# Kernel optimization log

Measured on AMD Instinct MI355X. Metric: run time of the kernel, lower is better.

The kernel has to match this reference:

```python
import jax, jax.numpy as jnp
import numpy as np

N_NODES = 50000
N_EDGES = 800000
IN_FEATS = 64
HIDDEN = 64
NUM_CLASSES = 8


def setup_inputs() -> dict:
    key = jax.random.key(0)
    ks = jax.random.split(key, 6)
    embeds = jax.random.normal(ks[0], (N_NODES, IN_FEATS), dtype=jnp.float32)
    edge_index = jax.random.randint(ks[1], (2, N_EDGES), 0, N_NODES, dtype=jnp.int32)
    sc1 = 1.0 / np.sqrt(IN_FEATS)
    sc2 = 1.0 / np.sqrt(HIDDEN)
    W_l1 = jax.random.normal(ks[2], (IN_FEATS, HIDDEN), dtype=jnp.float32) * sc1
    b_l1 = jnp.zeros((HIDDEN,), dtype=jnp.float32)
    W_r1 = jax.random.normal(ks[3], (IN_FEATS, HIDDEN), dtype=jnp.float32) * sc1
    W_l2 = jax.random.normal(ks[4], (HIDDEN, NUM_CLASSES), dtype=jnp.float32) * sc2
    b_l2 = jnp.zeros((NUM_CLASSES,), dtype=jnp.float32)
    W_r2 = jax.random.normal(ks[5], (HIDDEN, NUM_CLASSES), dtype=jnp.float32) * sc2
    return {"embeds": embeds, "edge_index": edge_index,
            "W_l1": W_l1, "b_l1": b_l1, "W_r1": W_r1,
            "W_l2": W_l2, "b_l2": b_l2, "W_r2": W_r2}


def _sage_conv(x, src, dst, W_l, b_l, W_r):
    # PyG SAGEConv('mean'): lin_l(mean_{j->i} x_j) + lin_r(x_i); lin_r has no bias.
    msg = x[src]                                                   # [E, F] gather
    agg = jax.ops.segment_sum(msg, dst, num_segments=N_NODES)      # [N, F]
    deg = jax.ops.segment_sum(jnp.ones((src.shape[0],), x.dtype), dst,
                              num_segments=N_NODES)                # [N]
    agg = agg / jnp.maximum(deg, 1.0)[:, None]
    return agg @ W_l + b_l + x @ W_r


def reference(embeds, edge_index, W_l1, b_l1, W_r1, W_l2, b_l2, W_r2):
    src, dst = edge_index[0], edge_index[1]
    h = _sage_conv(embeds, src, dst, W_l1, b_l1, W_r1)
    # dropout between layers is identity at inference; source applies no ReLU
    h = _sage_conv(h, src, dst, W_l2, b_l2, W_r2)
    return h
```

## Files before the change

### kernel.cpp

```cpp
#include <hip/hip_runtime.h>
#include <hip/hip_bf16.h>
#include <cstddef>

#define N_FEATS 64
#define NBKT_SHIFT 8
#define EPB 4096
#define CAP 6144

typedef __attribute__((ext_vector_type(8))) short bf16x8;
typedef __attribute__((ext_vector_type(4))) float f32x4;

__device__ __forceinline__ unsigned f2bf(float f) {
    unsigned x = __float_as_uint(f);
    return (x + 0x7fffu + ((x >> 16) & 1u)) >> 16;
}

__global__ __launch_bounds__(256) void k_init(
        const float* __restrict__ Wl1, const float* __restrict__ bl1,
        const float* __restrict__ Wr1, const float* __restrict__ Wl2,
        const float* __restrict__ bl2, const float* __restrict__ Wr2,
        unsigned short* __restrict__ Wc, float* __restrict__ bvec,
        int* __restrict__ cursor, int nbkt) {
    int tid = threadIdx.x;
    int k = tid & 63, jg = tid >> 6;
    const float* W1 = (jg < 2) ? Wl1 : Wr1;
    const float* W2 = (jg & 1) ? Wr2 : Wl2;
    float acc[8] = {0.f,0.f,0.f,0.f,0.f,0.f,0.f,0.f};
    for (int m = 0; m < 64; ++m) {
        float w1 = W1[k * 64 + m];
        #pragma unroll
        for (int jj = 0; jj < 8; ++jj) acc[jj] += w1 * W2[m * 8 + jj];
    }
    #pragma unroll
    for (int jj = 0; jj < 8; ++jj)
        Wc[k * 32 + jg * 8 + jj] = (unsigned short)f2bf(acc[jj]);
    if (tid < 16) {
        const float* W2b = (tid < 8) ? Wl2 : Wr2;
        float a = 0.f;
        for (int m = 0; m < 64; ++m) a += bl1[m] * W2b[m * 8 + (tid & 7)];
        if (tid >= 8) a += bl2[tid - 8];
        bvec[tid] = a;
    }
    if (tid < nbkt) cursor[tid] = 0;
}

__global__ __launch_bounds__(256) void k_split_gemm(
        const int* __restrict__ src, const int* __restrict__ dst,
        int* __restrict__ cursor, unsigned* __restrict__ pairs,
        int nEdges, int nbkt, int nb1,
        const float* __restrict__ x,
        const unsigned short* __restrict__ Wc,
        const float* __restrict__ bvec,
        unsigned short* __restrict__ G,
        float* __restrict__ T,
        int nNodes, int nStrips) {
    __shared__ unsigned spr[EPB];
    __shared__ int lh[256];
    __shared__ int lcur[256];
    int tid = threadIdx.x, b = blockIdx.x;

    if (b < nb1) {
        lh[tid] = 0;
        __syncthreads();
        int base = b * EPB;
        int m = nEdges - base; if (m > EPB) m = EPB;
        for (int j = tid; j < m; j += 256) {
            unsigned d = (unsigned)dst[base + j];
            spr[j] = ((unsigned)src[base + j] << 16) | d;
            atomicAdd(&lh[d >> NBKT_SHIFT], 1);
        }
        __syncthreads();
        if (tid < nbkt) lcur[tid] = atomicAdd(&cursor[tid], lh[tid]);
        __syncthreads();
        for (int j = tid; j < m; j += 256) {
            unsigned pr = spr[j];
            unsigned d = pr & 0xffffu;
            int bkt = d >> NBKT_SHIFT;
            int pos = atomicAdd(&lcur[bkt], 1);
            if (pos < CAP)
                pairs[(size_t)bkt * CAP + pos] = ((pr >> 16) << 8) | (d & 255u);
        }
        return;
    }

    int w  = tid >> 6;
    int l  = tid & 63;
    int fc = l & 15;
    int kg = l >> 4;
    bf16x8 bf[2][2];
    #pragma unroll
    for (int ct = 0; ct < 2; ++ct)
        #pragma unroll
        for (int kh = 0; kh < 2; ++kh)
            #pragma unroll
            for (int i = 0; i < 8; ++i) {
                int k = kh * 32 + kg * 8 + i;
                bf[ct][kh][i] = (short)Wc[k * 32 + ct * 16 + fc];
            }
    float bias = bvec[fc];

    for (int strip = b - nb1; strip < nStrips; strip += gridDim.x - nb1) {
        int node0 = strip * 64;
        int arow = node0 + w * 16 + fc;
        int ar = (arow < nNodes) ? arow : (nNodes - 1);
        const float* xp = x + (size_t)ar * 64 + kg * 8;
        float4 xa = *(const float4*)(xp);
        float4 xb = *(const float4*)(xp + 4);
        float4 xc = *(const float4*)(xp + 32);
        float4 xd = *(const float4*)(xp + 36);
        bf16x8 a0, a1;
        a0[0]=(short)f2bf(xa.x); a0[1]=(short)f2bf(xa.y);
        a0[2]=(short)f2bf(xa.z); a0[3]=(short)f2bf(xa.w);
        a0[4]=(short)f2bf(xb.x); a0[5]=(short)f2bf(xb.y);
        a0[6]=(short)f2bf(xb.z); a0[7]=(short)f2bf(xb.w);
        a1[0]=(short)f2bf(xc.x); a1[1]=(short)f2bf(xc.y);
        a1[2]=(short)f2bf(xc.z); a1[3]=(short)f2bf(xc.w);
        a1[4]=(short)f2bf(xd.x); a1[5]=(short)f2bf(xd.y);
        a1[6]=(short)f2bf(xd.z); a1[7]=(short)f2bf(xd.w);

        f32x4 d0 = {0.f, 0.f, 0.f, 0.f};
        f32x4 d1 = {0.f, 0.f, 0.f, 0.f};
        d0 = __builtin_amdgcn_mfma_f32_16x16x32_bf16(a0, bf[0][0], d0, 0, 0, 0);
        d0 = __builtin_amdgcn_mfma_f32_16x16x32_bf16(a1, bf[0][1], d0, 0, 0, 0);
        d1 = __builtin_amdgcn_mfma_f32_16x16x32_bf16(a0, bf[1][0], d1, 0, 0, 0);
        d1 = __builtin_amdgcn_mfma_f32_16x16x32_bf16(a1, bf[1][1], d1, 0, 0, 0);

        #pragma unroll
        for (int r = 0; r < 4; ++r) {
            int node = node0 + w * 16 + kg * 4 + r;
            if (node < nNodes) {
                G[(size_t)node * 16 + fc] = (unsigned short)f2bf(d0[r]);
                T[(size_t)node * 16 + fc] = d1[r] + bias;
            }
        }
    }
}

__global__ __launch_bounds__(1024) void k_fsort_gather2(
        const unsigned* __restrict__ pairs,
        const int* __restrict__ cursor,
        const unsigned* __restrict__ G,
        const float* __restrict__ T,
        int* __restrict__ counts,
        int* __restrict__ offsets,
        unsigned short* __restrict__ sorted_src,
        unsigned* __restrict__ pbf,
        float* __restrict__ q,
        int nNodes, int nbkt) {
    __shared__ unsigned short ss[CAP];
    __shared__ int cntA[256];
    __shared__ int scanbuf[256];
    __shared__ int loff[256];
    __shared__ int cur[256];
    int tid = threadIdx.x, b = blockIdx.x;
    int bStart = b * CAP;
    int m = cursor[b]; if (m > CAP) m = CAP;

    if (tid < 256) cntA[tid] = 0;
    __syncthreads();
    for (int e = tid; e < m; e += 1024)
        atomicAdd(&cntA[pairs[bStart + e] & 255u], 1);
    __syncthreads();
    int v = 0;
    if (tid < 256) { v = cntA[tid]; scanbuf[tid] = v; }
    __syncthreads();
    for (int d = 1; d < 256; d <<= 1) {
        int t = (tid < 256 && tid >= d) ? scanbuf[tid - d] : 0;
        __syncthreads();
        if (tid < 256) scanbuf[tid] += t;
        __syncthreads();
    }
    if (tid < 256) {
        int excl = scanbuf[tid] - v;
        loff[tid] = excl;
        cur[tid] = excl;
        int node = (b << NBKT_SHIFT) + tid;
        if (node < nNodes) { counts[node] = v; offsets[node] = bStart + excl; }
    }
    __syncthreads();
    for (int e = tid; e < m; e += 1024) {
        unsigned pr = pairs[bStart + e];
        int pos = atomicAdd(&cur[pr & 255u], 1);
        unsigned short sv = (unsigned short)(pr >> 8);
        ss[pos] = sv;
        sorted_src[bStart + pos] = sv;
    }
    __syncthreads();

    int wave = tid >> 6, lane = tid & 63;
    int half = lane >> 5;
    int eg   = (lane >> 2) & 7;
    int t4   = lane & 3;
    const uint2* G2 = (const uint2*)G;

    #pragma unroll 1
    for (int it = 0; it < 8; ++it) {
        int nl = it * 32 + wave * 2 + half;
        int node = (b << NBKT_SHIFT) + nl;
        if (node >= nNodes) continue;
        int cnt_n = cntA[nl];
        int lo = loff[nl];

        float a0 = 0.f, a1 = 0.f, a2 = 0.f, a3 = 0.f;
        int id = (eg < cnt_n) ? (int)ss[lo + eg] : -1;
        for (int base = 0; base < cnt_n; base += 8) {
            int en = base + 8 + eg;
            int idn = (en < cnt_n) ? (int)ss[lo + en] : -1;
            if (id >= 0) {
                uint2 r = G2[(size_t)id * 4 + t4];
                a0 += __uint_as_float(r.x << 16);
                a1 += __uint_as_float(r.x & 0xffff0000u);
                a2 += __uint_as_float(r.y << 16);
                a3 += __uint_as_float(r.y & 0xffff0000u);
            }
            id = idn;
        }
        a0 += __shfl_xor(a0, 4);  a1 += __shfl_xor(a1, 4);
        a2 += __shfl_xor(a2, 4);  a3 += __shfl_xor(a3, 4);
        a0 += __shfl_xor(a0, 8);  a1 += __shfl_xor(a1, 8);
        a2 += __shfl_xor(a2, 8);  a3 += __shfl_xor(a3, 8);
        a0 += __shfl_xor(a0, 16); a1 += __shfl_xor(a1, 16);
        a2 += __shfl_xor(a2, 16); a3 += __shfl_xor(a3, 16);

        if (eg == 0) {
            float inv = 1.0f / fmaxf((float)cnt_n, 1.0f);
            float4 tv = *(const float4*)&T[(size_t)node * 16 + t4 * 4];
            float r0 = a0 * inv + tv.x;
            float r1 = a1 * inv + tv.y;
            float r2 = a2 * inv + tv.z;
            float r3 = a3 * inv + tv.w;
            if (t4 < 2) {
                uint2 o;
                o.x = f2bf(r0) | (f2bf(r1) << 16);
                o.y = f2bf(r2) | (f2bf(r3) << 16);
                *(uint2*)(pbf + (size_t)node * 4 + t4 * 2) = o;
            } else {
                float4 o; o.x = r0; o.y = r1; o.z = r2; o.w = r3;
                *(float4*)(q + (size_t)node * 8 + (t4 - 2) * 4) = o;
            }
        }
    }
}

__global__ __launch_bounds__(256) void k_final(
        const unsigned* __restrict__ pbf,
        const float* __restrict__ q,
        const int* __restrict__ counts,
        const int* __restrict__ offsets,
        const unsigned short* __restrict__ ss,
        float* __restrict__ out,
        int nNodes) {
    int tid  = threadIdx.x;
    int wave = tid >> 6, lane = tid & 63;
    int half = lane >> 5;
    int eg   = (lane >> 1) & 15;
    int t2   = lane & 1;
    int node = blockIdx.x * 8 + wave * 2 + half;
    if (node >= nNodes) return;
    int cnt = counts[node], off = offsets[node];
    const uint2* P2 = (const uint2*)pbf;

    float a0 = 0.f, a1 = 0.f, a2 = 0.f, a3 = 0.f;
    int id = (eg < cnt) ? (int)ss[off + eg] : -1;
    for (int base = 0; base < cnt; base += 16) {
        int en = base + 16 + eg;
        int idn = (en < cnt) ? (int)ss[off + en] : -1;
        if (id >= 0) {
            uint2 r = P2[(size_t)id * 2 + t2];
            a0 += __uint_as_float(r.x << 16);
            a1 += __uint_as_float(r.x & 0xffff0000u);
            a2 += __uint_as_float(r.y << 16);
            a3 += __uint_as_float(r.y & 0xffff0000u);
        }
        id = idn;
    }
    a0 += __shfl_xor(a0, 2);  a1 += __shfl_xor(a1, 2);
    a2 += __shfl_xor(a2, 2);  a3 += __shfl_xor(a3, 2);
    a0 += __shfl_xor(a0, 4);  a1 += __shfl_xor(a1, 4);
    a2 += __shfl_xor(a2, 4);  a3 += __shfl_xor(a3, 4);
    a0 += __shfl_xor(a0, 8);  a1 += __shfl_xor(a1, 8);
    a2 += __shfl_xor(a2, 8);  a3 += __shfl_xor(a3, 8);
    a0 += __shfl_xor(a0, 16); a1 += __shfl_xor(a1, 16);
    a2 += __shfl_xor(a2, 16); a3 += __shfl_xor(a3, 16);

    if (eg == 0) {
        float inv = 1.0f / fmaxf((float)cnt, 1.0f);
        float4 qv = *(const float4*)&q[(size_t)node * 8 + t2 * 4];
        float4 o;
        o.x = a0 * inv + qv.x; o.y = a1 * inv + qv.y;
        o.z = a2 * inv + qv.z; o.w = a3 * inv + qv.w;
        *(float4*)(out + (size_t)node * 8 + t2 * 4) = o;
    }
}

static inline size_t align256(size_t v) { return (v + 255) & ~(size_t)255; }

extern "C" void kernel_launch(void* const* d_in, const int* in_sizes, int n_in,
                              void* d_out, int out_size, void* d_ws, size_t ws_size,
                              hipStream_t stream) {
    const float* embeds = (const float*)d_in[0];
    const int*   ei     = (const int*)d_in[1];
    const float* Wl1    = (const float*)d_in[2];
    const float* bl1    = (const float*)d_in[3];
    const float* Wr1    = (const float*)d_in[4];
    const float* Wl2    = (const float*)d_in[5];
    const float* bl2    = (const float*)d_in[6];
    const float* Wr2    = (const float*)d_in[7];

    const int N = in_sizes[0] / N_FEATS;
    const int E = in_sizes[1] / 2;
    const int* src = ei;
    const int* dst = ei + E;

    const int NBKT = (N + 255) >> NBKT_SHIFT;
    const int NB1  = (E + EPB - 1) / EPB;
    const int NSTRIPS = (N + 63) / 64;

    char* ws = (char*)d_ws;
    size_t off = 0;
    int*            cursor     = (int*)(ws + off); off += align256((size_t)NBKT * sizeof(int));
    int*            counts     = (int*)(ws + off); off += align256((size_t)N * sizeof(int));
    int*            offsets    = (int*)(ws + off); off += align256((size_t)N * sizeof(int));
    unsigned short* Wc         = (unsigned short*)(ws + off); off += align256(64 * 32 * sizeof(unsigned short));
    float*          bvec       = (float*)(ws + off); off += align256(16 * sizeof(float));
    unsigned*       pairs      = (unsigned*)(ws + off); off += align256((size_t)NBKT * CAP * sizeof(unsigned));
    unsigned short* sorted_src = (unsigned short*)(ws + off); off += align256((size_t)NBKT * CAP * sizeof(unsigned short));
    unsigned*       G          = (unsigned*)(ws + off); off += align256((size_t)N * 16 * sizeof(unsigned short));
    float*          T          = (float*)(ws + off); off += align256((size_t)N * 16 * sizeof(float));
    unsigned*       pbf        = (unsigned*)(ws + off); off += align256((size_t)N * 4 * sizeof(unsigned));
    float*          q          = (float*)(ws + off); off += align256((size_t)N * 8 * sizeof(float));
    (void)ws_size;

    k_init<<<1, 256, 0, stream>>>(Wl1, bl1, Wr1, Wl2, bl2, Wr2, Wc, bvec,
                                  cursor, NBKT);
    k_split_gemm<<<NB1 + NSTRIPS, 256, 0, stream>>>(
        src, dst, cursor, pairs, E, NBKT, NB1,
        embeds, Wc, bvec, (unsigned short*)G, T, N, NSTRIPS);
    k_fsort_gather2<<<NBKT, 1024, 0, stream>>>(
        pairs, cursor, G, T, counts, offsets, sorted_src, pbf, q, N, NBKT);
    k_final<<<(N + 7) / 8, 256, 0, stream>>>(pbf, q, counts, offsets, sorted_src,
                                             (float*)d_out, N);
}
```

Baseline: 62.91 us.

## Fold weight-product init into GEMM blocks and use 8 lanes-per-node in final gather

The separate single-block k_init kernel is removed. Each GEMM block now recomputes the combined W1·W2 bf16 weights and bias into shared memory, and a memset zeroes the bucket cursors, which saves one launch and its serial dependency. k_final now assigns 16 nodes per block with 8 edge-groups per node instead of 16, so lanes are used better given the average degree of about 16, and one shuffle stage is dropped. The trade-off is redundant weight-product work in every GEMM block (64x64x8 per block) and a memset call in place of the kernel.

```diff
diff --git a/kernel.cpp b/kernel.cpp
--- a/kernel.cpp
+++ b/kernel.cpp
@@ -13,35 +13,6 @@
 __device__ __forceinline__ unsigned f2bf(float f) {
     unsigned x = __float_as_uint(f);
     return (x + 0x7fffu + ((x >> 16) & 1u)) >> 16;
-}
-
-__global__ __launch_bounds__(256) void k_init(
-        const float* __restrict__ Wl1, const float* __restrict__ bl1,
-        const float* __restrict__ Wr1, const float* __restrict__ Wl2,
-        const float* __restrict__ bl2, const float* __restrict__ Wr2,
-        unsigned short* __restrict__ Wc, float* __restrict__ bvec,
-        int* __restrict__ cursor, int nbkt) {
-    int tid = threadIdx.x;
-    int k = tid & 63, jg = tid >> 6;
-    const float* W1 = (jg < 2) ? Wl1 : Wr1;
-    const float* W2 = (jg & 1) ? Wr2 : Wl2;
-    float acc[8] = {0.f,0.f,0.f,0.f,0.f,0.f,0.f,0.f};
-    for (int m = 0; m < 64; ++m) {
-        float w1 = W1[k * 64 + m];
-        #pragma unroll
-        for (int jj = 0; jj < 8; ++jj) acc[jj] += w1 * W2[m * 8 + jj];
-    }
-    #pragma unroll
-    for (int jj = 0; jj < 8; ++jj)
-        Wc[k * 32 + jg * 8 + jj] = (unsigned short)f2bf(acc[jj]);
-    if (tid < 16) {
-        const float* W2b = (tid < 8) ? Wl2 : Wr2;
-        float a = 0.f;
-        for (int m = 0; m < 64; ++m) a += bl1[m] * W2b[m * 8 + (tid & 7)];
-        if (tid >= 8) a += bl2[tid - 8];
-        bvec[tid] = a;
-    }
-    if (tid < nbkt) cursor[tid] = 0;
 }
 
 __global__ __launch_bounds__(256) void k_split_gemm(
@@ -49,14 +20,17 @@
         int* __restrict__ cursor, unsigned* __restrict__ pairs,
         int nEdges, int nbkt, int nb1,
         const float* __restrict__ x,
-        const unsigned short* __restrict__ Wc,
-        const float* __restrict__ bvec,
+        const float* __restrict__ Wl1, const float* __restrict__ bl1,
+        const float* __restrict__ Wr1, const float* __restrict__ Wl2,
+        const float* __restrict__ bl2, const float* __restrict__ Wr2,
         unsigned short* __restrict__ G,
         float* __restrict__ T,
         int nNodes, int nStrips) {
     __shared__ unsigned spr[EPB];
     __shared__ int lh[256];
     __shared__ int lcur[256];
+    __shared__ unsigned short sWc[64 * 32];
+    __shared__ float sbv[16];
     int tid = threadIdx.x, b = blockIdx.x;
 
     if (b < nb1) {
@@ -82,6 +56,29 @@
         }
         return;
     }
+
+    {
+        int k = tid & 63, jg = tid >> 6;
+        const float* W1 = (jg < 2) ? Wl1 : Wr1;
+        const float* W2 = (jg & 1) ? Wr2 : Wl2;
+        float acc[8] = {0.f,0.f,0.f,0.f,0.f,0.f,0.f,0.f};
+        for (int m = 0; m < 64; ++m) {
+            float w1 = W1[k * 64 + m];
+            #pragma unroll
+            for (int jj = 0; jj < 8; ++jj) acc[jj] += w1 * W2[m * 8 + jj];
+        }
+        #pragma unroll
+        for (int jj = 0; jj < 8; ++jj)
+            sWc[k * 32 + jg * 8 + jj] = (unsigned short)f2bf(acc[jj]);
+        if (tid < 16) {
+            const float* W2b = (tid < 8) ? Wl2 : Wr2;
+            float a = 0.f;
+            for (int m = 0; m < 64; ++m) a += bl1[m] * W2b[m * 8 + (tid & 7)];
+            if (tid >= 8) a += bl2[tid - 8];
+            sbv[tid] = a;
+        }
+    }
+    __syncthreads();
 
     int w  = tid >> 6;
     int l  = tid & 63;
@@ -95,9 +92,9 @@
             #pragma unroll
             for (int i = 0; i < 8; ++i) {
                 int k = kh * 32 + kg * 8 + i;
-                bf[ct][kh][i] = (short)Wc[k * 32 + ct * 16 + fc];
+                bf[ct][kh][i] = (short)sWc[k * 32 + ct * 16 + fc];
             }
-    float bias = bvec[fc];
+    float bias = sbv[fc];
 
     for (int strip = b - nb1; strip < nStrips; strip += gridDim.x - nb1) {
         int node0 = strip * 64;
@@ -252,18 +249,18 @@
         int nNodes) {
     int tid  = threadIdx.x;
     int wave = tid >> 6, lane = tid & 63;
-    int half = lane >> 5;
-    int eg   = (lane >> 1) & 15;
+    int quarter = lane >> 4;
+    int eg   = (lane >> 1) & 7;
     int t2   = lane & 1;
-    int node = blockIdx.x * 8 + wave * 2 + half;
+    int node = blockIdx.x * 16 + wave * 4 + quarter;
     if (node >= nNodes) return;
     int cnt = counts[node], off = offsets[node];
     const uint2* P2 = (const uint2*)pbf;
 
     float a0 = 0.f, a1 = 0.f, a2 = 0.f, a3 = 0.f;
     int id = (eg < cnt) ? (int)ss[off + eg] : -1;
-    for (int base = 0; base < cnt; base += 16) {
-        int en = base + 16 + eg;
+    for (int base = 0; base < cnt; base += 8) {
+        int en = base + 8 + eg;
         int idn = (en < cnt) ? (int)ss[off + en] : -1;
         if (id >= 0) {
             uint2 r = P2[(size_t)id * 2 + t2];
@@ -280,8 +277,6 @@
     a2 += __shfl_xor(a2, 4);  a3 += __shfl_xor(a3, 4);
     a0 += __shfl_xor(a0, 8);  a1 += __shfl_xor(a1, 8);
     a2 += __shfl_xor(a2, 8);  a3 += __shfl_xor(a3, 8);
-    a0 += __shfl_xor(a0, 16); a1 += __shfl_xor(a1, 16);
-    a2 += __shfl_xor(a2, 16); a3 += __shfl_xor(a3, 16);
 
     if (eg == 0) {
         float inv = 1.0f / fmaxf((float)cnt, 1.0f);
@@ -321,8 +316,6 @@
     int*            cursor     = (int*)(ws + off); off += align256((size_t)NBKT * sizeof(int));
     int*            counts     = (int*)(ws + off); off += align256((size_t)N * sizeof(int));
     int*            offsets    = (int*)(ws + off); off += align256((size_t)N * sizeof(int));
-    unsigned short* Wc         = (unsigned short*)(ws + off); off += align256(64 * 32 * sizeof(unsigned short));
-    float*          bvec       = (float*)(ws + off); off += align256(16 * sizeof(float));
     unsigned*       pairs      = (unsigned*)(ws + off); off += align256((size_t)NBKT * CAP * sizeof(unsigned));
     unsigned short* sorted_src = (unsigned short*)(ws + off); off += align256((size_t)NBKT * CAP * sizeof(unsigned short));
     unsigned*       G          = (unsigned*)(ws + off); off += align256((size_t)N * 16 * sizeof(unsigned short));
@@ -331,13 +324,13 @@
     float*          q          = (float*)(ws + off); off += align256((size_t)N * 8 * sizeof(float));
     (void)ws_size;
 
-    k_init<<<1, 256, 0, stream>>>(Wl1, bl1, Wr1, Wl2, bl2, Wr2, Wc, bvec,
-                                  cursor, NBKT);
+    hipMemsetAsync(cursor, 0, (size_t)NBKT * sizeof(int), stream);
     k_split_gemm<<<NB1 + NSTRIPS, 256, 0, stream>>>(
         src, dst, cursor, pairs, E, NBKT, NB1,
-        embeds, Wc, bvec, (unsigned short*)G, T, N, NSTRIPS);
+        embeds, Wl1, bl1, Wr1, Wl2, bl2, Wr2,
+        (unsigned short*)G, T, N, NSTRIPS);
     k_fsort_gather2<<<NBKT, 1024, 0, stream>>>(
         pairs, cursor, G, T, counts, offsets, sorted_src, pbf, q, N, NBKT);
-    k_final<<<(N + 7) / 8, 256, 0, stream>>>(pbf, q, counts, offsets, sorted_src,
-                                             (float*)d_out, N);
-}
+    k_final<<<(N + 15) / 16, 256, 0, stream>>>(pbf, q, counts, offsets,
+                                               sorted_src, (float*)d_out, N);
+}
```

Measured after the change: 71.25 us. +13.3%, slower.

## Fuse second-layer gather into sort kernel via grid-wide atomic barrier

Applied to the files above, without the earlier changes.

Merges the final aggregation kernel into the sort/gather kernel. A software grid barrier (atomic counter spin) separates the two layers, and the second layer reuses the sorted source lists already held in shared memory. This removes one kernel launch and the global writes and reads of counts, offsets and sorted_src. The cost is that the final gather now runs on only 196 blocks of 1024 threads instead of many small blocks, and the spin barrier assumes all blocks are co-resident, so it could deadlock if they are not.

```diff
diff --git a/kernel.cpp b/kernel.cpp
--- a/kernel.cpp
+++ b/kernel.cpp
@@ -20,7 +20,7 @@
         const float* __restrict__ Wr1, const float* __restrict__ Wl2,
         const float* __restrict__ bl2, const float* __restrict__ Wr2,
         unsigned short* __restrict__ Wc, float* __restrict__ bvec,
-        int* __restrict__ cursor, int nbkt) {
+        int* __restrict__ cursor, int* __restrict__ barrier, int nbkt) {
     int tid = threadIdx.x;
     int k = tid & 63, jg = tid >> 6;
     const float* W1 = (jg < 2) ? Wl1 : Wr1;
@@ -42,6 +42,7 @@
         bvec[tid] = a;
     }
     if (tid < nbkt) cursor[tid] = 0;
+    if (tid == 0) *barrier = 0;
 }
 
 __global__ __launch_bounds__(256) void k_split_gemm(
@@ -136,16 +137,15 @@
     }
 }
 
-__global__ __launch_bounds__(1024) void k_fsort_gather2(
+__global__ __launch_bounds__(1024) void k_fg_final(
         const unsigned* __restrict__ pairs,
         const int* __restrict__ cursor,
         const unsigned* __restrict__ G,
         const float* __restrict__ T,
-        int* __restrict__ counts,
-        int* __restrict__ offsets,
-        unsigned short* __restrict__ sorted_src,
         unsigned* __restrict__ pbf,
         float* __restrict__ q,
+        int* __restrict__ barrier,
+        float* __restrict__ out,
         int nNodes, int nbkt) {
     __shared__ unsigned short ss[CAP];
     __shared__ int cntA[256];
@@ -174,122 +174,126 @@
         int excl = scanbuf[tid] - v;
         loff[tid] = excl;
         cur[tid] = excl;
-        int node = (b << NBKT_SHIFT) + tid;
-        if (node < nNodes) { counts[node] = v; offsets[node] = bStart + excl; }
     }
     __syncthreads();
     for (int e = tid; e < m; e += 1024) {
         unsigned pr = pairs[bStart + e];
         int pos = atomicAdd(&cur[pr & 255u], 1);
-        unsigned short sv = (unsigned short)(pr >> 8);
-        ss[pos] = sv;
-        sorted_src[bStart + pos] = sv;
+        ss[pos] = (unsigned short)(pr >> 8);
     }
     __syncthreads();
 
     int wave = tid >> 6, lane = tid & 63;
-    int half = lane >> 5;
-    int eg   = (lane >> 2) & 7;
-    int t4   = lane & 3;
-    const uint2* G2 = (const uint2*)G;
-
-    #pragma unroll 1
-    for (int it = 0; it < 8; ++it) {
-        int nl = it * 32 + wave * 2 + half;
-        int node = (b << NBKT_SHIFT) + nl;
-        if (node >= nNodes) continue;
-        int cnt_n = cntA[nl];
-        int lo = loff[nl];
-
-        float a0 = 0.f, a1 = 0.f, a2 = 0.f, a3 = 0.f;
-        int id = (eg < cnt_n) ? (int)ss[lo + eg] : -1;
-        for (int base = 0; base < cnt_n; base += 8) {
-            int en = base + 8 + eg;
-            int idn = (en < cnt_n) ? (int)ss[lo + en] : -1;
-            if (id >= 0) {
-                uint2 r = G2[(size_t)id * 4 + t4];
-                a0 += __uint_as_float(r.x << 16);
-                a1 += __uint_as_float(r.x & 0xffff0000u);
-                a2 += __uint_as_float(r.y << 16);
-                a3 += __uint_as_float(r.y & 0xffff0000u);
-            }
-            id = idn;
-        }
-        a0 += __shfl_xor(a0, 4);  a1 += __shfl_xor(a1, 4);
-        a2 += __shfl_xor(a2, 4);  a3 += __shfl_xor(a3, 4);
-        a0 += __shfl_xor(a0, 8);  a1 += __shfl_xor(a1, 8);
-        a2 += __shfl_xor(a2, 8);  a3 += __shfl_xor(a3, 8);
-        a0 += __shfl_xor(a0, 16); a1 += __shfl_xor(a1, 16);
-        a2 += __shfl_xor(a2, 16); a3 += __shfl_xor(a3, 16);
-
-        if (eg == 0) {
-            float inv = 1.0f / fmaxf((float)cnt_n, 1.0f);
-            float4 tv = *(const float4*)&T[(size_t)node * 16 + t4 * 4];
-            float r0 = a0 * inv + tv.x;
-            float r1 = a1 * inv + tv.y;
-            float r2 = a2 * inv + tv.z;
-            float r3 = a3 * inv + tv.w;
-            if (t4 < 2) {
-                uint2 o;
-                o.x = f2bf(r0) | (f2bf(r1) << 16);
-                o.y = f2bf(r2) | (f2bf(r3) << 16);
-                *(uint2*)(pbf + (size_t)node * 4 + t4 * 2) = o;
-            } else {
-                float4 o; o.x = r0; o.y = r1; o.z = r2; o.w = r3;
-                *(float4*)(q + (size_t)node * 8 + (t4 - 2) * 4) = o;
-            }
-        }
-    }
-}
-
-__global__ __launch_bounds__(256) void k_final(
-        const unsigned* __restrict__ pbf,
-        const float* __restrict__ q,
-        const int* __restrict__ counts,
-        const int* __restrict__ offsets,
-        const unsigned short* __restrict__ ss,
-        float* __restrict__ out,
-        int nNodes) {
-    int tid  = threadIdx.x;
-    int wave = tid >> 6, lane = tid & 63;
-    int half = lane >> 5;
-    int eg   = (lane >> 1) & 15;
-    int t2   = lane & 1;
-    int node = blockIdx.x * 8 + wave * 2 + half;
-    if (node >= nNodes) return;
-    int cnt = counts[node], off = offsets[node];
-    const uint2* P2 = (const uint2*)pbf;
-
-    float a0 = 0.f, a1 = 0.f, a2 = 0.f, a3 = 0.f;
-    int id = (eg < cnt) ? (int)ss[off + eg] : -1;
-    for (int base = 0; base < cnt; base += 16) {
-        int en = base + 16 + eg;
-        int idn = (en < cnt) ? (int)ss[off + en] : -1;
-        if (id >= 0) {
-            uint2 r = P2[(size_t)id * 2 + t2];
-            a0 += __uint_as_float(r.x << 16);
-            a1 += __uint_as_float(r.x & 0xffff0000u);
-            a2 += __uint_as_float(r.y << 16);
-            a3 += __uint_as_float(r.y & 0xffff0000u);
-        }
-        id = idn;
-    }
-    a0 += __shfl_xor(a0, 2);  a1 += __shfl_xor(a1, 2);
-    a2 += __shfl_xor(a2, 2);  a3 += __shfl_xor(a3, 2);
-    a0 += __shfl_xor(a0, 4);  a1 += __shfl_xor(a1, 4);
-    a2 += __shfl_xor(a2, 4);  a3 += __shfl_xor(a3, 4);
-    a0 += __shfl_xor(a0, 8);  a1 += __shfl_xor(a1, 8);
-    a2 += __shfl_xor(a2, 8);  a3 += __shfl_xor(a3, 8);
-    a0 += __shfl_xor(a0, 16); a1 += __shfl_xor(a1, 16);
-    a2 += __shfl_xor(a2, 16); a3 += __shfl_xor(a3, 16);
-
-    if (eg == 0) {
-        float inv = 1.0f / fmaxf((float)cnt, 1.0f);
-        float4 qv = *(const float4*)&q[(size_t)node * 8 + t2 * 4];
-        float4 o;
-        o.x = a0 * inv + qv.x; o.y = a1 * inv + qv.y;
-        o.z = a2 * inv + qv.z; o.w = a3 * inv + qv.w;
-        *(float4*)(out + (size_t)node * 8 + t2 * 4) = o;
+
+    {
+        int half = lane >> 5;
+        int eg   = (lane >> 2) & 7;
+        int t4   = lane & 3;
+        const uint2* G2 = (const uint2*)G;
+
+        #pragma unroll 1
+        for (int it = 0; it < 8; ++it) {
+            int nl = it * 32 + wave * 2 + half;
+            int node = (b << NBKT_SHIFT) + nl;
+            if (node >= nNodes) continue;
+            int cnt_n = cntA[nl];
+            int lo = loff[nl];
+
+            float a0 = 0.f, a1 = 0.f, a2 = 0.f, a3 = 0.f;
+            int id = (eg < cnt_n) ? (int)ss[lo + eg] : -1;
+            for (int base = 0; base < cnt_n; base += 8) {
+                int en = base + 8 + eg;
+                int idn = (en < cnt_n) ? (int)ss[lo + en] : -1;
+                if (id >= 0) {
+                    uint2 r = G2[(size_t)id * 4 + t4];
+                    a0 += __uint_as_float(r.x << 16);
+                    a1 += __uint_as_float(r.x & 0xffff0000u);
+                    a2 += __uint_as_float(r.y << 16);
+                    a3 += __uint_as_float(r.y & 0xffff0000u);
+                }
+                id = idn;
+            }
+            a0 += __shfl_xor(a0, 4);  a1 += __shfl_xor(a1, 4);
+            a2 += __shfl_xor(a2, 4);  a3 += __shfl_xor(a3, 4);
+            a0 += __shfl_xor(a0, 8);  a1 += __shfl_xor(a1, 8);
+            a2 += __shfl_xor(a2, 8);  a3 += __shfl_xor(a3, 8);
+            a0 += __shfl_xor(a0, 16); a1 += __shfl_xor(a1, 16);
+            a2 += __shfl_xor(a2, 16); a3 += __shfl_xor(a3, 16);
+
+            if (eg == 0) {
+                float inv = 1.0f / fmaxf((float)cnt_n, 1.0f);
+                float4 tv = *(const float4*)&T[(size_t)node * 16 + t4 * 4];
+                float r0 = a0 * inv + tv.x;
+                float r1 = a1 * inv + tv.y;
+                float r2 = a2 * inv + tv.z;
+                float r3 = a3 * inv + tv.w;
+                if (t4 < 2) {
+                    uint2 o;
+                    o.x = f2bf(r0) | (f2bf(r1) << 16);
+                    o.y = f2bf(r2) | (f2bf(r3) << 16);
+                    *(uint2*)(pbf + (size_t)node * 4 + t4 * 2) = o;
+                } else {
+                    float4 o; o.x = r0; o.y = r1; o.z = r2; o.w = r3;
+                    *(float4*)(q + (size_t)node * 8 + (t4 - 2) * 4) = o;
+                }
+            }
+        }
+    }
+
+    __threadfence();
+    __syncthreads();
+    if (tid == 0) {
+        atomicAdd(barrier, 1);
+        while (atomicAdd(barrier, 0) < nbkt) { }
+    }
+    __syncthreads();
+
+    {
+        int half = lane >> 5;
+        int eg   = (lane >> 1) & 15;
+        int t2   = lane & 1;
+        const uint2* P2 = (const uint2*)pbf;
+
+        #pragma unroll 1
+        for (int it = 0; it < 8; ++it) {
+            int nl = it * 32 + wave * 2 + half;
+            int node = (b << NBKT_SHIFT) + nl;
+            if (node >= nNodes) continue;
+            int cnt_n = cntA[nl];
+            int lo = loff[nl];
+
+            float a0 = 0.f, a1 = 0.f, a2 = 0.f, a3 = 0.f;
+            int id = (eg < cnt_n) ? (int)ss[lo + eg] : -1;
+            for (int base = 0; base < cnt_n; base += 16) {
+                int en = base + 16 + eg;
+                int idn = (en < cnt_n) ? (int)ss[lo + en] : -1;
+                if (id >= 0) {
+                    uint2 r = P2[(size_t)id * 2 + t2];
+                    a0 += __uint_as_float(r.x << 16);
+                    a1 += __uint_as_float(r.x & 0xffff0000u);
+                    a2 += __uint_as_float(r.y << 16);
+                    a3 += __uint_as_float(r.y & 0xffff0000u);
+                }
+                id = idn;
+            }
+            a0 += __shfl_xor(a0, 2);  a1 += __shfl_xor(a1, 2);
+            a2 += __shfl_xor(a2, 2);  a3 += __shfl_xor(a3, 2);
+            a0 += __shfl_xor(a0, 4);  a1 += __shfl_xor(a1, 4);
+            a2 += __shfl_xor(a2, 4);  a3 += __shfl_xor(a3, 4);
+            a0 += __shfl_xor(a0, 8);  a1 += __shfl_xor(a1, 8);
+            a2 += __shfl_xor(a2, 8);  a3 += __shfl_xor(a3, 8);
+            a0 += __shfl_xor(a0, 16); a1 += __shfl_xor(a1, 16);
+            a2 += __shfl_xor(a2, 16); a3 += __shfl_xor(a3, 16);
+
+            if (eg == 0) {
+                float inv = 1.0f / fmaxf((float)cnt_n, 1.0f);
+                float4 qv = *(const float4*)&q[(size_t)node * 8 + t2 * 4];
+                float4 o;
+                o.x = a0 * inv + qv.x; o.y = a1 * inv + qv.y;
+                o.z = a2 * inv + qv.z; o.w = a3 * inv + qv.w;
+                *(float4*)(out + (size_t)node * 8 + t2 * 4) = o;
+            }
+        }
     }
 }
 
@@ -318,26 +322,22 @@
 
     char* ws = (char*)d_ws;
     size_t off = 0;
-    int*            cursor     = (int*)(ws + off); off += align256((size_t)NBKT * sizeof(int));
-    int*            counts     = (int*)(ws + off); off += align256((size_t)N * sizeof(int));
-    int*            offsets    = (int*)(ws + off); off += align256((size_t)N * sizeof(int));
-    unsigned short* Wc         = (unsigned short*)(ws + off); off += align256(64 * 32 * sizeof(unsigned short));
-    float*          bvec       = (float*)(ws + off); off += align256(16 * sizeof(float));
-    unsigned*       pairs      = (unsigned*)(ws + off); off += align256((size_t)NBKT * CAP * sizeof(unsigned));
-    unsigned short* sorted_src = (unsigned short*)(ws + off); off += align256((size_t)NBKT * CAP * sizeof(unsigned short));
-    unsigned*       G          = (unsigned*)(ws + off); off += align256((size_t)N * 16 * sizeof(unsigned short));
-    float*          T          = (float*)(ws + off); off += align256((size_t)N * 16 * sizeof(float));
-    unsigned*       pbf        = (unsigned*)(ws + off); off += align256((size_t)N * 4 * sizeof(unsigned));
-    float*          q          = (float*)(ws + off); off += align256((size_t)N * 8 * sizeof(float));
+    int*            cursor  = (int*)(ws + off); off += align256((size_t)NBKT * sizeof(int));
+    int*            barrier = (int*)(ws + off); off += align256(sizeof(int));
+    unsigned short* Wc      = (unsigned short*)(ws + off); off += align256(64 * 32 * sizeof(unsigned short));
+    float*          bvec    = (float*)(ws + off); off += align256(16 * sizeof(float));
+    unsigned*       pairs   = (unsigned*)(ws + off); off += align256((size_t)NBKT * CAP * sizeof(unsigned));
+    unsigned*       G       = (unsigned*)(ws + off); off += align256((size_t)N * 16 * sizeof(unsigned short));
+    float*          T       = (float*)(ws + off); off += align256((size_t)N * 16 * sizeof(float));
+    unsigned*       pbf     = (unsigned*)(ws + off); off += align256((size_t)N * 4 * sizeof(unsigned));
+    float*          q       = (float*)(ws + off); off += align256((size_t)N * 8 * sizeof(float));
     (void)ws_size;
 
     k_init<<<1, 256, 0, stream>>>(Wl1, bl1, Wr1, Wl2, bl2, Wr2, Wc, bvec,
-                                  cursor, NBKT);
+                                  cursor, barrier, NBKT);
     k_split_gemm<<<NB1 + NSTRIPS, 256, 0, stream>>>(
         src, dst, cursor, pairs, E, NBKT, NB1,
         embeds, Wc, bvec, (unsigned short*)G, T, N, NSTRIPS);
-    k_fsort_gather2<<<NBKT, 1024, 0, stream>>>(
-        pairs, cursor, G, T, counts, offsets, sorted_src, pbf, q, N, NBKT);
-    k_final<<<(N + 7) / 8, 256, 0, stream>>>(pbf, q, counts, offsets, sorted_src,
-                                             (float*)d_out, N);
-}
+    k_fg_final<<<NBKT, 1024, 0, stream>>>(
+        pairs, cursor, G, T, pbf, q, barrier, (float*)d_out, N, NBKT);
+}
```

After: 125.5 us. 99.5% more time.
